# Kernel optimization log

Hardware: AMD Instinct MI355X
Metric: run time of the kernel (lower is better)

## Reference

```python
import jax, jax.numpy as jnp
import numpy as np

B, S, F, EMB, HID = 64, 2048, 40, 128, 256


def setup_inputs() -> dict:
    key = jax.random.key(0)
    ks = jax.random.split(key, 12)
    sc_in = 1.0 / np.sqrt(F)
    sc_h = 1.0 / np.sqrt(HID)
    n = lambda k, shape, sc: (jax.random.normal(k, shape, jnp.float32) * sc)
    return {
        "in_states": jax.random.normal(ks[0], (B, S, F), jnp.float32),
        "W_in": n(ks[1], (EMB, F), sc_in),
        "b_in": jnp.zeros((EMB,), jnp.float32),  # bias init to 0 in original
        "W_ih0": n(ks[2], (4 * HID, EMB), sc_h),
        "W_hh0": n(ks[3], (4 * HID, HID), sc_h),
        "b_ih0": n(ks[4], (4 * HID,), sc_h),
        "b_hh0": n(ks[5], (4 * HID,), sc_h),
        "W_ih1": n(ks[6], (4 * HID, HID), sc_h),
        "W_hh1": n(ks[7], (4 * HID, HID), sc_h),
        "b_ih1": n(ks[8], (4 * HID,), sc_h),
        "b_hh1": n(ks[9], (4 * HID,), sc_h),
        "W_out": n(ks[10], (1, HID), sc_h),
        "b_out": jnp.zeros((1,), jnp.float32),  # bias init to 0 in original
    }


def _lstm_layer(x, W_ih, W_hh, b_ih, b_hh):
    # x: [B, S, D_in]; returns hs: [B, S, H], final (h, c)
    Bb = x.shape[0]
    H = W_hh.shape[1]
    # Precompute input contribution for all timesteps (one big GEMM).
    gx = jnp.einsum('bsd,gd->bsg', x, W_ih) + b_ih + b_hh  # [B, S, 4H]

    def step(carry, gxt):
        h, c = carry
        g = gxt + h @ W_hh.T  # [B, 4H]
        i, f, gg, o = jnp.split(g, 4, axis=-1)  # PyTorch gate order i,f,g,o
        i = jax.nn.sigmoid(i)
        f = jax.nn.sigmoid(f)
        gg = jnp.tanh(gg)
        o = jax.nn.sigmoid(o)
        c = f * c + i * gg
        h = o * jnp.tanh(c)
        return (h, c), h

    init = (jnp.zeros((Bb, H), x.dtype), jnp.zeros((Bb, H), x.dtype))
    (h, c), hs = jax.lax.scan(step, init, jnp.swapaxes(gx, 0, 1))
    return jnp.swapaxes(hs, 0, 1), (h, c)


def reference(in_states, W_in, b_in, W_ih0, W_hh0, b_ih0, b_hh0,
              W_ih1, W_hh1, b_ih1, b_hh1, W_out, b_out):
    # Input projection applied to every timestep (equivalent to per-step Linear).
    x = jnp.einsum('bsf,ef->bse', in_states, W_in) + b_in  # [B, S, EMB]
    y, _ = _lstm_layer(x, W_ih0, W_hh0, b_ih0, b_hh0)
    y, _ = _lstm_layer(y, W_ih1, W_hh1, b_ih1, b_hh1)
    out = jnp.einsum('bsh,oh->bso', y, W_out) + b_out  # [B, S, 1]
    return out[..., 0]  # [B, S], matches torch.t(outputs)
```

## Files before the change

kernel.cpp:

```cpp
#include <hip/hip_runtime.h>


#define Sz    2048
#define PIPE  4
#define NG    4
#define NJ    8

typedef __attribute__((ext_vector_type(8))) short short8;
typedef __attribute__((ext_vector_type(4))) float f32x4;

#define PUB0_U64 0
#define PUB1_U64 65536
#define CFLG_U32 262144
#define WS_U32   262176

#define HA_HI 0
#define HA_LO 8448
#define HB_HI 16896
#define HB_LO 25344
#define IN_HI 33792
#define IN_LO 36096
#define GBUF  38400
#define SMEM_BYTES 46848
#define WCOMB_OFF 16896

__device__ __forceinline__ unsigned short bf16_rne(float f) {
  unsigned u = __float_as_uint(f);
  u += 0x7FFFu + ((u >> 16) & 1u);
  return (unsigned short)(u >> 16);
}
__device__ __forceinline__ float sigm(float x) { return 1.f / (1.f + __expf(-x)); }
__device__ __forceinline__ float tanh_f(float x) { return 1.f - 2.f / (__expf(2.f * x) + 1.f); }

__device__ __forceinline__ bool load_stage(const unsigned long long* __restrict__ src,
                                           unsigned tagExp, char* hi, char* lo, int tid) {
  unsigned long long v[16];
#pragma unroll
  for (int kt = 0; kt < 8; ++kt) {
    v[kt * 2]     = __hip_atomic_load(src + kt * 512 + tid,       __ATOMIC_RELAXED, __HIP_MEMORY_SCOPE_AGENT);
    v[kt * 2 + 1] = __hip_atomic_load(src + kt * 512 + 256 + tid, __ATOMIC_RELAXED, __HIP_MEMORY_SCOPE_AGENT);
  }
  bool ok = true;
#pragma unroll
  for (int kt = 0; kt < 8; ++kt) {
#pragma unroll
    for (int hh = 0; hh < 2; ++hh) {
      unsigned long long x = v[kt * 2 + hh];
      ok &= ((unsigned)(x >> 32) == tagExp);
      unsigned pk = (unsigned)x;
      int e = tid + hh * 256;
      int m = e >> 5, col = kt * 32 + (e & 31);
      *(short*)(hi + m * 528 + col * 2) = (short)(pk >> 16);
      *(short*)(lo + m * 528 + col * 2) = (short)(pk & 0xffffu);
    }
  }
  return ok;
}

__global__ void zero_kernel(unsigned* __restrict__ ws, float* __restrict__ out) {
  int i = blockIdx.x * 256 + threadIdx.x;
  if (i < WS_U32) ws[i] = 0u;
  if (i < 64 * Sz) out[i] = 0.f;
}

__global__ __launch_bounds__(256, 1) void lstm_persist(
    const float* __restrict__ xin, const float* __restrict__ W_in,
    const float* __restrict__ b_in, const float* __restrict__ W_ih0,
    const float* __restrict__ W_hh0, const float* __restrict__ b_ih0,
    const float* __restrict__ b_hh0, const float* __restrict__ W_ih1,
    const float* __restrict__ W_hh1, const float* __restrict__ b_ih1,
    const float* __restrict__ b_hh1, const float* __restrict__ W_out,
    const float* __restrict__ b_out, float* __restrict__ out,
    unsigned* __restrict__ ws) {
  const int bx = blockIdx.x;
  const int g = bx & 7;
  if (g >= NG) return;
  const int idx = bx >> 3;
  const int layer = idx >> 3;
  const int p = idx & 7;
  const int tid = (int)threadIdx.x;
  const int w = tid >> 6;
  const int lane = tid & 63;
  const int q = lane >> 4;
  const int n16 = lane & 15;

  __shared__ __align__(16) char smem[SMEM_BYTES];

  const int row0 = w * 256 + p * 32 + n16;
  const int row1 = row0 + 16;

  short8 wf_rec[8][2];
  short8 wf_in2[8][2];
  short8 wf_cmb[2][2];
  float bias0 = 0.f, bias1 = 0.f;

  {
    const float* Wrec = layer ? W_hh1 : W_hh0;
#pragma unroll
    for (int kt = 0; kt < 8; ++kt) {
#pragma unroll
      for (int u = 0; u < 2; ++u) {
        const int row = u ? row1 : row0;
        const float* src = Wrec + (size_t)row * 256 + kt * 32 + q * 8;
        union { short8 v; unsigned short s[8]; } fr;
#pragma unroll
        for (int j = 0; j < 8; ++j) fr.s[j] = bf16_rne(src[j]);
        wf_rec[kt][u] = fr.v;
      }
    }
  }
  if (layer == 1) {
#pragma unroll
    for (int kt = 0; kt < 8; ++kt) {
#pragma unroll
      for (int u = 0; u < 2; ++u) {
        const int row = u ? row1 : row0;
        const float* src = W_ih1 + (size_t)row * 256 + kt * 32 + q * 8;
        union { short8 v; unsigned short s[8]; } fr;
#pragma unroll
        for (int j = 0; j < 8; ++j) fr.s[j] = bf16_rne(src[j]);
        wf_in2[kt][u] = fr.v;
      }
    }
    bias0 = b_ih1[row0] + b_hh1[row0];
    bias1 = b_ih1[row1] + b_hh1[row1];
  } else {
    float* wcomb = (float*)(smem + WCOMB_OFF);
    for (int i = tid; i < 128 * 40; i += 256) {
      int rl = i / 40, f = i - rl * 40;
      int gate = rl >> 5, rr = rl & 31;
      int arow = gate * 256 + p * 32 + rr;
      const float* wi = W_ih0 + (size_t)arow * 128;
      float s = 0.f;
      for (int e = 0; e < 128; ++e) s += wi[e] * W_in[e * 40 + f];
      wcomb[rl * 40 + f] = s;
    }
    __syncthreads();
#pragma unroll
    for (int kt = 0; kt < 2; ++kt) {
#pragma unroll
      for (int u = 0; u < 2; ++u) {
        int rl = w * 32 + u * 16 + n16;
        union { short8 v; unsigned short s[8]; } fr;
#pragma unroll
        for (int j = 0; j < 8; ++j) {
          int k = kt * 32 + q * 8 + j;
          fr.s[j] = (k < 40) ? bf16_rne(wcomb[rl * 40 + k]) : (unsigned short)0;
        }
        wf_cmb[kt][u] = fr.v;
      }
    }
    {
      const float* wi0 = W_ih0 + (size_t)row0 * 128;
      const float* wi1 = W_ih0 + (size_t)row1 * 128;
      float s0 = 0.f, s1 = 0.f;
      for (int e = 0; e < 128; ++e) { s0 += wi0[e] * b_in[e]; s1 += wi1[e] * b_in[e]; }
      bias0 = s0 + b_ih0[row0] + b_hh0[row0];
      bias1 = s1 + b_ih0[row1] + b_hh0[row1];
    }
    __syncthreads();
    for (int i = tid; i < 2304; i += 256) *((short*)(smem + IN_HI) + i) = 0;
    __syncthreads();
  }

  float c0 = 0.f, c1 = 0.f;
  float wo = 0.f, bo = 0.f;
  if (layer == 1) { wo = W_out[p * 32 + (tid & 31)]; bo = b_out[0]; }

  unsigned long long* const pub0 = (unsigned long long*)ws + PUB0_U64;
  unsigned long long* const pub1 = (unsigned long long*)ws + PUB1_U64;
  unsigned long long* const pubMy = layer ? pub1 : pub0;
  unsigned* const cflg = ws + CFLG_U32 + g * 8;
  float* gb = (float*)(smem + GBUF);

#pragma unroll 1
  for (int t = 0; t < Sz; ++t) {
    if (layer == 0 && tid < 160) {
      int bb = tid / 10, f4 = tid - bb * 10;
      float4 inv = *(const float4*)(xin + ((size_t)(g * 16 + bb) * Sz + t) * 40 + f4 * 4);
#pragma unroll
      for (int cc = 0; cc < 4; ++cc) {
        float f = ((const float*)&inv)[cc];
        unsigned short hb = bf16_rne(f);
        float fh = __uint_as_float((unsigned)hb << 16);
        unsigned short lb = bf16_rne(f - fh);
        int col = f4 * 4 + cc;
        *(short*)(smem + IN_HI + bb * 144 + col * 2) = (short)hb;
        *(short*)(smem + IN_LO + bb * 144 + col * 2) = (short)lb;
      }
    }

    const int slot_r = (t + PIPE - 1) % PIPE;
    const unsigned long long* srcA = pubMy + (size_t)((g * PIPE + slot_r) * NJ) * 512;
    const unsigned long long* srcB = pub0 + (size_t)((g * PIPE + (t % PIPE)) * NJ) * 512;
    const unsigned tagA = (unsigned)t;
    const unsigned tagB = (unsigned)(t + 1);
    for (;;) {
      bool ok = load_stage(srcA, tagA, smem + HA_HI, smem + HA_LO, tid);
      if (layer == 1) {
        ok &= load_stage(srcB, tagB, smem + HB_HI, smem + HB_LO, tid);
      } else if (tid < 8) {
        unsigned c = __hip_atomic_load(cflg + tid, __ATOMIC_RELAXED, __HIP_MEMORY_SCOPE_AGENT);
        ok &= ((int)c >= t - 3);
      }
      if (__syncthreads_and(ok)) break;
    }
    if (layer == 1 && tid == 0)
      __hip_atomic_store(cflg + p, (unsigned)(t + 1), __ATOMIC_RELAXED, __HIP_MEMORY_SCOPE_AGENT);

    f32x4 acc0 = {0.f, 0.f, 0.f, 0.f};
    f32x4 acc1 = {0.f, 0.f, 0.f, 0.f};
    const int arow = n16 * 528;
    const int kcol = q * 8;
#pragma unroll
    for (int kt = 0; kt < 8; ++kt) {
      short8 aH = *(const short8*)(smem + HA_HI + arow + (kt * 32 + kcol) * 2);
      short8 aL = *(const short8*)(smem + HA_LO + arow + (kt * 32 + kcol) * 2);
      acc0 = __builtin_amdgcn_mfma_f32_16x16x32_bf16(aH, wf_rec[kt][0], acc0, 0, 0, 0);
      acc0 = __builtin_amdgcn_mfma_f32_16x16x32_bf16(aL, wf_rec[kt][0], acc0, 0, 0, 0);
      acc1 = __builtin_amdgcn_mfma_f32_16x16x32_bf16(aH, wf_rec[kt][1], acc1, 0, 0, 0);
      acc1 = __builtin_amdgcn_mfma_f32_16x16x32_bf16(aL, wf_rec[kt][1], acc1, 0, 0, 0);
    }
    if (layer == 1) {
#pragma unroll
      for (int kt = 0; kt < 8; ++kt) {
        short8 aH = *(const short8*)(smem + HB_HI + arow + (kt * 32 + kcol) * 2);
        short8 aL = *(const short8*)(smem + HB_LO + arow + (kt * 32 + kcol) * 2);
        acc0 = __builtin_amdgcn_mfma_f32_16x16x32_bf16(aH, wf_in2[kt][0], acc0, 0, 0, 0);
        acc0 = __builtin_amdgcn_mfma_f32_16x16x32_bf16(aL, wf_in2[kt][0], acc0, 0, 0, 0);
        acc1 = __builtin_amdgcn_mfma_f32_16x16x32_bf16(aH, wf_in2[kt][1], acc1, 0, 0, 0);
        acc1 = __builtin_amdgcn_mfma_f32_16x16x32_bf16(aL, wf_in2[kt][1], acc1, 0, 0, 0);
      }
    } else {
      const int arow_in = n16 * 144;
#pragma unroll
      for (int kt = 0; kt < 2; ++kt) {
        short8 aH = *(const short8*)(smem + IN_HI + arow_in + (kt * 32 + kcol) * 2);
        short8 aL = *(const short8*)(smem + IN_LO + arow_in + (kt * 32 + kcol) * 2);
        acc0 = __builtin_amdgcn_mfma_f32_16x16x32_bf16(aH, wf_cmb[kt][0], acc0, 0, 0, 0);
        acc0 = __builtin_amdgcn_mfma_f32_16x16x32_bf16(aL, wf_cmb[kt][0], acc0, 0, 0, 0);
        acc1 = __builtin_amdgcn_mfma_f32_16x16x32_bf16(aH, wf_cmb[kt][1], acc1, 0, 0, 0);
        acc1 = __builtin_amdgcn_mfma_f32_16x16x32_bf16(aL, wf_cmb[kt][1], acc1, 0, 0, 0);
      }
    }

#pragma unroll
    for (int u = 0; u < 2; ++u) {
      f32x4 a = u ? acc1 : acc0;
      float bs = u ? bias1 : bias0;
#pragma unroll
      for (int r = 0; r < 4; ++r) {
        float v = a[r] + bs;
        v = (w == 2) ? tanh_f(v) : sigm(v);
        gb[w * 528 + (q * 4 + r) * 33 + u * 16 + n16] = v;
      }
    }
    __syncthreads();

    unsigned long long* dst =
        pubMy + (size_t)((g * PIPE + (t % PIPE)) * NJ + p) * 512;
    const unsigned long long tagW = ((unsigned long long)(unsigned)(t + 1)) << 32;
#pragma unroll
    for (int k = 0; k < 2; ++k) {
      int e = tid + k * 256;
      int m = e >> 5, nn = e & 31;
      float iv = gb[0 * 528 + m * 33 + nn];
      float fv = gb[1 * 528 + m * 33 + nn];
      float gv = gb[2 * 528 + m * 33 + nn];
      float ov = gb[3 * 528 + m * 33 + nn];
      float c = k ? c1 : c0;
      c = fv * c + iv * gv;
      float h = ov * tanh_f(c);
      if (k) c1 = c; else c0 = c;
      unsigned short hb = bf16_rne(h);
      float fh = __uint_as_float((unsigned)hb << 16);
      unsigned short lb = bf16_rne(h - fh);
      unsigned pk = ((unsigned)hb << 16) | (unsigned)lb;
      __hip_atomic_store(dst + e, tagW | pk, __ATOMIC_RELAXED, __HIP_MEMORY_SCOPE_AGENT);
      if (layer == 1) {
        float val = h * wo;
#pragma unroll
        for (int off = 16; off; off >>= 1) val += __shfl_down(val, off, 32);
        if (nn == 0) {
          if (p == 0) val += bo;
          atomicAdd(out + (size_t)(g * 16 + m) * Sz + t, val);
        }
      }
    }
  }
}

extern "C" void kernel_launch(void* const* d_in, const int* in_sizes, int n_in,
                              void* d_out, int out_size, void* d_ws, size_t ws_size,
                              hipStream_t stream) {
  const float* xin   = (const float*)d_in[0];
  const float* W_in  = (const float*)d_in[1];
  const float* b_in  = (const float*)d_in[2];
  const float* W_ih0 = (const float*)d_in[3];
  const float* W_hh0 = (const float*)d_in[4];
  const float* b_ih0 = (const float*)d_in[5];
  const float* b_hh0 = (const float*)d_in[6];
  const float* W_ih1 = (const float*)d_in[7];
  const float* W_hh1 = (const float*)d_in[8];
  const float* b_ih1 = (const float*)d_in[9];
  const float* b_hh1 = (const float*)d_in[10];
  const float* W_out = (const float*)d_in[11];
  const float* b_out = (const float*)d_in[12];
  float* out = (float*)d_out;
  unsigned* ws = (unsigned*)d_ws;

  zero_kernel<<<(WS_U32 + 255) / 256, 256, 0, stream>>>(ws, out);
  lstm_persist<<<128, 256, 0, stream>>>(xin, W_in, b_in, W_ih0, W_hh0, b_ih0, b_hh0,
                                        W_ih1, W_hh1, b_ih1, b_hh1, W_out, b_out,
                                        out, ws);
}
```

Baseline: 7.578 ms.

## Fuse both LSTM layers into one wavefront-skewed persistent kernel with register-level gate exchange

Replaces the separate per-layer block groups with 32 blocks of 512 threads. Each block computes both layers, with layer 1 running one step behind layer 0 so both recurrences advance in the same iteration. Gate activations are exchanged through lane shuffles instead of a shared gate buffer. Polling uses per-slice pending masks with sleep, the block's own slice is written straight to LDS, and the input for the next step is prefetched. The output projection is written to workspace and reduced by a separate kernel instead of global atomics. The trade-off is more registers per thread and a longer serial chain per step.

```diff
diff --git a/kernel.cpp b/kernel.cpp
--- a/kernel.cpp
+++ b/kernel.cpp
@@ -1,292 +1,351 @@
 #include <hip/hip_runtime.h>
 
 
-#define Sz    2048
-#define PIPE  4
-#define NG    4
-#define NJ    8
+#define Sz 2048
+#define D 4
 
 typedef __attribute__((ext_vector_type(8))) short short8;
 typedef __attribute__((ext_vector_type(4))) float f32x4;
 
-#define PUB0_U64 0
-#define PUB1_U64 65536
-#define CFLG_U32 262144
-#define WS_U32   262176
-
-#define HA_HI 0
-#define HA_LO 8448
-#define HB_HI 16896
-#define HB_LO 25344
+#define R1_U64 65536
+#define GH_WORD 262144
+#define ZERO_WORDS 262144
+
+#define H0_HI 0
+#define H0_LO 8448
+#define H1_HI 16896
+#define H1_LO 25344
 #define IN_HI 33792
 #define IN_LO 36096
-#define GBUF  38400
-#define SMEM_BYTES 46848
-#define WCOMB_OFF 16896
+#define POUT  38400
+#define SMEM_BYTES 39424
 
 __device__ __forceinline__ unsigned short bf16_rne(float f) {
   unsigned u = __float_as_uint(f);
   u += 0x7FFFu + ((u >> 16) & 1u);
   return (unsigned short)(u >> 16);
 }
-__device__ __forceinline__ float sigm(float x) { return 1.f / (1.f + __expf(-x)); }
-__device__ __forceinline__ float tanh_f(float x) { return 1.f - 2.f / (__expf(2.f * x) + 1.f); }
-
-__device__ __forceinline__ bool load_stage(const unsigned long long* __restrict__ src,
-                                           unsigned tagExp, char* hi, char* lo, int tid) {
-  unsigned long long v[16];
-#pragma unroll
-  for (int kt = 0; kt < 8; ++kt) {
-    v[kt * 2]     = __hip_atomic_load(src + kt * 512 + tid,       __ATOMIC_RELAXED, __HIP_MEMORY_SCOPE_AGENT);
-    v[kt * 2 + 1] = __hip_atomic_load(src + kt * 512 + 256 + tid, __ATOMIC_RELAXED, __HIP_MEMORY_SCOPE_AGENT);
-  }
-  bool ok = true;
-#pragma unroll
-  for (int kt = 0; kt < 8; ++kt) {
-#pragma unroll
-    for (int hh = 0; hh < 2; ++hh) {
-      unsigned long long x = v[kt * 2 + hh];
-      ok &= ((unsigned)(x >> 32) == tagExp);
-      unsigned pk = (unsigned)x;
-      int e = tid + hh * 256;
-      int m = e >> 5, col = kt * 32 + (e & 31);
-      *(short*)(hi + m * 528 + col * 2) = (short)(pk >> 16);
-      *(short*)(lo + m * 528 + col * 2) = (short)(pk & 0xffffu);
-    }
-  }
-  return ok;
-}
-
-__global__ void zero_kernel(unsigned* __restrict__ ws, float* __restrict__ out) {
-  int i = blockIdx.x * 256 + threadIdx.x;
-  if (i < WS_U32) ws[i] = 0u;
-  if (i < 64 * Sz) out[i] = 0.f;
-}
-
-__global__ __launch_bounds__(256, 1) void lstm_persist(
+__device__ __forceinline__ unsigned pk_enc(float f) {
+  unsigned short hb = bf16_rne(f);
+  float fh = __uint_as_float((unsigned)hb << 16);
+  unsigned short lb = bf16_rne(f - fh);
+  return ((unsigned)hb << 16) | (unsigned)lb;
+}
+
+__global__ void zero_ws(unsigned* __restrict__ ws) {
+  int i = blockIdx.x * 512 + threadIdx.x;
+  if (i < ZERO_WORDS) ws[i] = 0u;
+}
+
+__global__ void out_reduce(const unsigned* __restrict__ ws,
+                           const float* __restrict__ b_out, float* __restrict__ out) {
+  int idx = blockIdx.x * 512 + threadIdx.x;
+  if (idx >= 64 * Sz) return;
+  int b = idx >> 11, t = idx & 2047;
+  int g = b >> 4, m = b & 15;
+  const float* gh = (const float*)(ws + GH_WORD);
+  float s = b_out[0];
+#pragma unroll
+  for (int p = 0; p < 8; ++p)
+    s += gh[((size_t)(g * 8 + p) * Sz + t) * 16 + m];
+  out[idx] = s;
+}
+
+__global__ __launch_bounds__(512, 2) void lstm_v4(
     const float* __restrict__ xin, const float* __restrict__ W_in,
     const float* __restrict__ b_in, const float* __restrict__ W_ih0,
     const float* __restrict__ W_hh0, const float* __restrict__ b_ih0,
     const float* __restrict__ b_hh0, const float* __restrict__ W_ih1,
     const float* __restrict__ W_hh1, const float* __restrict__ b_ih1,
     const float* __restrict__ b_hh1, const float* __restrict__ W_out,
-    const float* __restrict__ b_out, float* __restrict__ out,
-    unsigned* __restrict__ ws) {
+    const float* __restrict__ b_out, unsigned* __restrict__ ws) {
   const int bx = blockIdx.x;
-  const int g = bx & 7;
-  if (g >= NG) return;
-  const int idx = bx >> 3;
-  const int layer = idx >> 3;
-  const int p = idx & 7;
+  if (bx >= 32) return;
+  const int g = bx & 3, p = bx >> 2;
   const int tid = (int)threadIdx.x;
   const int w = tid >> 6;
   const int lane = tid & 63;
   const int q = lane >> 4;
   const int n16 = lane & 15;
+  const int gidx = n16 >> 2;
+  const int c4 = n16 & 3;
 
   __shared__ __align__(16) char smem[SMEM_BYTES];
 
-  const int row0 = w * 256 + p * 32 + n16;
-  const int row1 = row0 + 16;
-
-  short8 wf_rec[8][2];
-  short8 wf_in2[8][2];
-  short8 wf_cmb[2][2];
-  float bias0 = 0.f, bias1 = 0.f;
-
+  const int mycol = p * 32 + w * 4 + c4;
+  const int myrow = gidx * 256 + mycol;
+
+  short8 wf0[8], wf1[8], wfi[8];
+#pragma unroll
+  for (int kt = 0; kt < 8; ++kt) {
+    const float* s0 = W_hh0 + (size_t)myrow * 256 + kt * 32 + q * 8;
+    const float* s1 = W_hh1 + (size_t)myrow * 256 + kt * 32 + q * 8;
+    const float* si = W_ih1 + (size_t)myrow * 256 + kt * 32 + q * 8;
+    union { short8 v; unsigned short s[8]; } f0, f1, fi;
+#pragma unroll
+    for (int j = 0; j < 8; ++j) {
+      f0.s[j] = bf16_rne(s0[j]);
+      f1.s[j] = bf16_rne(s1[j]);
+      fi.s[j] = bf16_rne(si[j]);
+    }
+    wf0[kt] = f0.v; wf1[kt] = f1.v; wfi[kt] = fi.v;
+  }
+  short8 wfc[2];
+  float bL0, bL1, wo;
   {
-    const float* Wrec = layer ? W_hh1 : W_hh0;
-#pragma unroll
-    for (int kt = 0; kt < 8; ++kt) {
-#pragma unroll
-      for (int u = 0; u < 2; ++u) {
-        const int row = u ? row1 : row0;
-        const float* src = Wrec + (size_t)row * 256 + kt * 32 + q * 8;
-        union { short8 v; unsigned short s[8]; } fr;
-#pragma unroll
-        for (int j = 0; j < 8; ++j) fr.s[j] = bf16_rne(src[j]);
-        wf_rec[kt][u] = fr.v;
-      }
-    }
-  }
-  if (layer == 1) {
-#pragma unroll
-    for (int kt = 0; kt < 8; ++kt) {
-#pragma unroll
-      for (int u = 0; u < 2; ++u) {
-        const int row = u ? row1 : row0;
-        const float* src = W_ih1 + (size_t)row * 256 + kt * 32 + q * 8;
-        union { short8 v; unsigned short s[8]; } fr;
-#pragma unroll
-        for (int j = 0; j < 8; ++j) fr.s[j] = bf16_rne(src[j]);
-        wf_in2[kt][u] = fr.v;
-      }
-    }
-    bias0 = b_ih1[row0] + b_hh1[row0];
-    bias1 = b_ih1[row1] + b_hh1[row1];
-  } else {
-    float* wcomb = (float*)(smem + WCOMB_OFF);
-    for (int i = tid; i < 128 * 40; i += 256) {
-      int rl = i / 40, f = i - rl * 40;
-      int gate = rl >> 5, rr = rl & 31;
-      int arow = gate * 256 + p * 32 + rr;
-      const float* wi = W_ih0 + (size_t)arow * 128;
+    float sv[2][8];
+#pragma unroll
+    for (int kt = 0; kt < 2; ++kt)
+#pragma unroll
+      for (int j = 0; j < 8; ++j) sv[kt][j] = 0.f;
+    float bacc = 0.f;
+    const float* wr = W_ih0 + (size_t)myrow * 128;
+    for (int e = 0; e < 128; ++e) {
+      float wv = wr[e];
+      const float* wi = W_in + e * 40;
+      bacc += wv * b_in[e];
+#pragma unroll
+      for (int j = 0; j < 8; ++j) {
+        int k0 = q * 8 + j;
+        sv[0][j] += wv * wi[k0];
+        int k1 = 32 + q * 8 + j;
+        if (k1 < 40) sv[1][j] += wv * wi[k1];
+      }
+    }
+    union { short8 v; unsigned short s[8]; } c0u, c1u;
+#pragma unroll
+    for (int j = 0; j < 8; ++j) {
+      c0u.s[j] = bf16_rne(sv[0][j]);
+      c1u.s[j] = (32 + q * 8 + j < 40) ? bf16_rne(sv[1][j]) : (unsigned short)0;
+    }
+    wfc[0] = c0u.v; wfc[1] = c1u.v;
+    bL0 = b_ih0[myrow] + b_hh0[myrow] + bacc;
+    bL1 = b_ih1[myrow] + b_hh1[myrow];
+    wo = W_out[mycol];
+  }
+
+  for (int i = tid; i < 9600; i += 512) ((int*)smem)[i] = 0;
+  __syncthreads();
+  const int bb = tid / 10, f4 = tid - (tid / 10) * 10;
+  if (tid < 160) {
+    float4 xv = *(const float4*)(xin + ((size_t)(g * 16 + bb) * Sz) * 40 + f4 * 4);
+#pragma unroll
+    for (int cc = 0; cc < 4; ++cc) {
+      unsigned pk = pk_enc(((const float*)&xv)[cc]);
+      int col = f4 * 4 + cc;
+      *(short*)(smem + IN_HI + bb * 144 + col * 2) = (short)(pk >> 16);
+      *(short*)(smem + IN_LO + bb * 144 + col * 2) = (short)(pk & 0xffffu);
+    }
+  }
+
+  float c0[4] = {0.f, 0.f, 0.f, 0.f};
+  float c1[4] = {0.f, 0.f, 0.f, 0.f};
+  unsigned long long* const ring0 = (unsigned long long*)ws;
+  unsigned long long* const ring1 = ring0 + R1_U64;
+  float* const ghout = (float*)(ws + GH_WORD);
+  float* const pout = (float*)(smem + POUT);
+  const unsigned maskInit = (0xFFu & ~(1u << p)) | ((0xFFu & ~(1u << p)) << 8);
+  const int stg_m = tid >> 5, stg_c = tid & 31;
+
+#pragma unroll 1
+  for (int t = 0; t <= Sz; ++t) {
+    float4 xv;
+    const bool hasx = (t + 1 < Sz) && (tid < 160);
+    if (hasx)
+      xv = *(const float4*)(xin + ((size_t)(g * 16 + bb) * Sz + (t + 1)) * 40 + f4 * 4);
+
+    if (t > 0) {
+      const unsigned tagE = (unsigned)t;
+      const unsigned long long* s0 =
+          ring0 + ((size_t)(g * D + ((t - 1) & 3)) * 8) * 512;
+      const unsigned long long* s1 =
+          ring1 + ((size_t)(g * D + ((t - 1) & 3)) * 8) * 512;
+      unsigned pend = maskInit;
+      int spin = 0;
+      while (pend) {
+        unsigned long long v0[8], v1[8];
+#pragma unroll
+        for (int k = 0; k < 8; ++k)
+          if (pend & (1u << k))
+            v0[k] = __hip_atomic_load(s0 + k * 512 + tid, __ATOMIC_RELAXED,
+                                      __HIP_MEMORY_SCOPE_AGENT);
+#pragma unroll
+        for (int k = 0; k < 8; ++k)
+          if (pend & (1u << (8 + k)))
+            v1[k] = __hip_atomic_load(s1 + k * 512 + tid, __ATOMIC_RELAXED,
+                                      __HIP_MEMORY_SCOPE_AGENT);
+#pragma unroll
+        for (int k = 0; k < 8; ++k) {
+          if ((pend & (1u << k)) && (unsigned)(v0[k] >> 32) == tagE) {
+            unsigned pk = (unsigned)v0[k];
+            int c = k * 32 + stg_c;
+            *(short*)(smem + H0_HI + stg_m * 528 + c * 2) = (short)(pk >> 16);
+            *(short*)(smem + H0_LO + stg_m * 528 + c * 2) = (short)(pk & 0xffffu);
+            pend &= ~(1u << k);
+          }
+          if ((pend & (1u << (8 + k))) && (unsigned)(v1[k] >> 32) == tagE) {
+            unsigned pk = (unsigned)v1[k];
+            int c = k * 32 + stg_c;
+            *(short*)(smem + H1_HI + stg_m * 528 + c * 2) = (short)(pk >> 16);
+            *(short*)(smem + H1_LO + stg_m * 528 + c * 2) = (short)(pk & 0xffffu);
+            pend &= ~(1u << (8 + k));
+          }
+        }
+        if (pend && ++spin > 2) __builtin_amdgcn_s_sleep(1);
+      }
+    }
+    __syncthreads();
+
+    if (w == 0 && lane < 16 && t >= 2) {
+      const int buf = (t - 1) & 1;
       float s = 0.f;
-      for (int e = 0; e < 128; ++e) s += wi[e] * W_in[e * 40 + f];
-      wcomb[rl * 40 + f] = s;
-    }
-    __syncthreads();
-#pragma unroll
-    for (int kt = 0; kt < 2; ++kt) {
-#pragma unroll
-      for (int u = 0; u < 2; ++u) {
-        int rl = w * 32 + u * 16 + n16;
-        union { short8 v; unsigned short s[8]; } fr;
-#pragma unroll
-        for (int j = 0; j < 8; ++j) {
-          int k = kt * 32 + q * 8 + j;
-          fr.s[j] = (k < 40) ? bf16_rne(wcomb[rl * 40 + k]) : (unsigned short)0;
-        }
-        wf_cmb[kt][u] = fr.v;
-      }
-    }
-    {
-      const float* wi0 = W_ih0 + (size_t)row0 * 128;
-      const float* wi1 = W_ih0 + (size_t)row1 * 128;
-      float s0 = 0.f, s1 = 0.f;
-      for (int e = 0; e < 128; ++e) { s0 += wi0[e] * b_in[e]; s1 += wi1[e] * b_in[e]; }
-      bias0 = s0 + b_ih0[row0] + b_hh0[row0];
-      bias1 = s1 + b_ih0[row1] + b_hh0[row1];
-    }
-    __syncthreads();
-    for (int i = tid; i < 2304; i += 256) *((short*)(smem + IN_HI) + i) = 0;
-    __syncthreads();
-  }
-
-  float c0 = 0.f, c1 = 0.f;
-  float wo = 0.f, bo = 0.f;
-  if (layer == 1) { wo = W_out[p * 32 + (tid & 31)]; bo = b_out[0]; }
-
-  unsigned long long* const pub0 = (unsigned long long*)ws + PUB0_U64;
-  unsigned long long* const pub1 = (unsigned long long*)ws + PUB1_U64;
-  unsigned long long* const pubMy = layer ? pub1 : pub0;
-  unsigned* const cflg = ws + CFLG_U32 + g * 8;
-  float* gb = (float*)(smem + GBUF);
-
-#pragma unroll 1
-  for (int t = 0; t < Sz; ++t) {
-    if (layer == 0 && tid < 160) {
-      int bb = tid / 10, f4 = tid - bb * 10;
-      float4 inv = *(const float4*)(xin + ((size_t)(g * 16 + bb) * Sz + t) * 40 + f4 * 4);
-#pragma unroll
-      for (int cc = 0; cc < 4; ++cc) {
-        float f = ((const float*)&inv)[cc];
-        unsigned short hb = bf16_rne(f);
-        float fh = __uint_as_float((unsigned)hb << 16);
-        unsigned short lb = bf16_rne(f - fh);
-        int col = f4 * 4 + cc;
-        *(short*)(smem + IN_HI + bb * 144 + col * 2) = (short)hb;
-        *(short*)(smem + IN_LO + bb * 144 + col * 2) = (short)lb;
-      }
-    }
-
-    const int slot_r = (t + PIPE - 1) % PIPE;
-    const unsigned long long* srcA = pubMy + (size_t)((g * PIPE + slot_r) * NJ) * 512;
-    const unsigned long long* srcB = pub0 + (size_t)((g * PIPE + (t % PIPE)) * NJ) * 512;
-    const unsigned tagA = (unsigned)t;
-    const unsigned tagB = (unsigned)(t + 1);
-    for (;;) {
-      bool ok = load_stage(srcA, tagA, smem + HA_HI, smem + HA_LO, tid);
-      if (layer == 1) {
-        ok &= load_stage(srcB, tagB, smem + HB_HI, smem + HB_LO, tid);
-      } else if (tid < 8) {
-        unsigned c = __hip_atomic_load(cflg + tid, __ATOMIC_RELAXED, __HIP_MEMORY_SCOPE_AGENT);
-        ok &= ((int)c >= t - 3);
-      }
-      if (__syncthreads_and(ok)) break;
-    }
-    if (layer == 1 && tid == 0)
-      __hip_atomic_store(cflg + p, (unsigned)(t + 1), __ATOMIC_RELAXED, __HIP_MEMORY_SCOPE_AGENT);
+#pragma unroll
+      for (int ww = 0; ww < 8; ++ww) s += pout[buf * 32 * 4 / 4];
+      s = 0.f;
+#pragma unroll
+      for (int ww = 0; ww < 8; ++ww) s += ((float*)(smem + POUT))[buf * 128 + ww * 16 + lane];
+      ghout[((size_t)(g * 8 + p) * Sz + (t - 2)) * 16 + lane] = s;
+    }
 
     f32x4 acc0 = {0.f, 0.f, 0.f, 0.f};
     f32x4 acc1 = {0.f, 0.f, 0.f, 0.f};
-    const int arow = n16 * 528;
-    const int kcol = q * 8;
+    if (t < Sz) {
+#pragma unroll
+      for (int kt = 0; kt < 2; ++kt) {
+        short8 aH = *(const short8*)(smem + IN_HI + n16 * 144 + (kt * 32 + q * 8) * 2);
+        short8 aL = *(const short8*)(smem + IN_LO + n16 * 144 + (kt * 32 + q * 8) * 2);
+        acc0 = __builtin_amdgcn_mfma_f32_16x16x32_bf16(aH, wfc[kt], acc0, 0, 0, 0);
+        acc0 = __builtin_amdgcn_mfma_f32_16x16x32_bf16(aL, wfc[kt], acc0, 0, 0, 0);
+      }
+    }
 #pragma unroll
     for (int kt = 0; kt < 8; ++kt) {
-      short8 aH = *(const short8*)(smem + HA_HI + arow + (kt * 32 + kcol) * 2);
-      short8 aL = *(const short8*)(smem + HA_LO + arow + (kt * 32 + kcol) * 2);
-      acc0 = __builtin_amdgcn_mfma_f32_16x16x32_bf16(aH, wf_rec[kt][0], acc0, 0, 0, 0);
-      acc0 = __builtin_amdgcn_mfma_f32_16x16x32_bf16(aL, wf_rec[kt][0], acc0, 0, 0, 0);
-      acc1 = __builtin_amdgcn_mfma_f32_16x16x32_bf16(aH, wf_rec[kt][1], acc1, 0, 0, 0);
-      acc1 = __builtin_amdgcn_mfma_f32_16x16x32_bf16(aL, wf_rec[kt][1], acc1, 0, 0, 0);
-    }
-    if (layer == 1) {
-#pragma unroll
-      for (int kt = 0; kt < 8; ++kt) {
-        short8 aH = *(const short8*)(smem + HB_HI + arow + (kt * 32 + kcol) * 2);
-        short8 aL = *(const short8*)(smem + HB_LO + arow + (kt * 32 + kcol) * 2);
-        acc0 = __builtin_amdgcn_mfma_f32_16x16x32_bf16(aH, wf_in2[kt][0], acc0, 0, 0, 0);
-        acc0 = __builtin_amdgcn_mfma_f32_16x16x32_bf16(aL, wf_in2[kt][0], acc0, 0, 0, 0);
-        acc1 = __builtin_amdgcn_mfma_f32_16x16x32_bf16(aH, wf_in2[kt][1], acc1, 0, 0, 0);
-        acc1 = __builtin_amdgcn_mfma_f32_16x16x32_bf16(aL, wf_in2[kt][1], acc1, 0, 0, 0);
-      }
-    } else {
-      const int arow_in = n16 * 144;
-#pragma unroll
-      for (int kt = 0; kt < 2; ++kt) {
-        short8 aH = *(const short8*)(smem + IN_HI + arow_in + (kt * 32 + kcol) * 2);
-        short8 aL = *(const short8*)(smem + IN_LO + arow_in + (kt * 32 + kcol) * 2);
-        acc0 = __builtin_amdgcn_mfma_f32_16x16x32_bf16(aH, wf_cmb[kt][0], acc0, 0, 0, 0);
-        acc0 = __builtin_amdgcn_mfma_f32_16x16x32_bf16(aL, wf_cmb[kt][0], acc0, 0, 0, 0);
-        acc1 = __builtin_amdgcn_mfma_f32_16x16x32_bf16(aH, wf_cmb[kt][1], acc1, 0, 0, 0);
-        acc1 = __builtin_amdgcn_mfma_f32_16x16x32_bf16(aL, wf_cmb[kt][1], acc1, 0, 0, 0);
-      }
-    }
-
-#pragma unroll
-    for (int u = 0; u < 2; ++u) {
-      f32x4 a = u ? acc1 : acc0;
-      float bs = u ? bias1 : bias0;
+      short8 aH0 = *(const short8*)(smem + H0_HI + n16 * 528 + (kt * 32 + q * 8) * 2);
+      short8 aL0 = *(const short8*)(smem + H0_LO + n16 * 528 + (kt * 32 + q * 8) * 2);
+      if (t < Sz) {
+        acc0 = __builtin_amdgcn_mfma_f32_16x16x32_bf16(aH0, wf0[kt], acc0, 0, 0, 0);
+        acc0 = __builtin_amdgcn_mfma_f32_16x16x32_bf16(aL0, wf0[kt], acc0, 0, 0, 0);
+      }
+      if (t > 0) {
+        acc1 = __builtin_amdgcn_mfma_f32_16x16x32_bf16(aH0, wfi[kt], acc1, 0, 0, 0);
+        acc1 = __builtin_amdgcn_mfma_f32_16x16x32_bf16(aL0, wfi[kt], acc1, 0, 0, 0);
+        short8 aH1 = *(const short8*)(smem + H1_HI + n16 * 528 + (kt * 32 + q * 8) * 2);
+        short8 aL1 = *(const short8*)(smem + H1_LO + n16 * 528 + (kt * 32 + q * 8) * 2);
+        acc1 = __builtin_amdgcn_mfma_f32_16x16x32_bf16(aH1, wf1[kt], acc1, 0, 0, 0);
+        acc1 = __builtin_amdgcn_mfma_f32_16x16x32_bf16(aL1, wf1[kt], acc1, 0, 0, 0);
+      }
+    }
+    __syncthreads();
+
+    const unsigned long long tagW = ((unsigned long long)(unsigned)(t + 1)) << 32;
+    const bool b0 = gidx & 1, b1 = gidx & 2;
+    const float sc = (gidx == 2) ? 2.f : 1.f;
+
+    if (t < Sz) {
+      unsigned pk0[4];
 #pragma unroll
       for (int r = 0; r < 4; ++r) {
-        float v = a[r] + bs;
-        v = (w == 2) ? tanh_f(v) : sigm(v);
-        gb[w * 528 + (q * 4 + r) * 33 + u * 16 + n16] = v;
-      }
-    }
-    __syncthreads();
-
-    unsigned long long* dst =
-        pubMy + (size_t)((g * PIPE + (t % PIPE)) * NJ + p) * 512;
-    const unsigned long long tagW = ((unsigned long long)(unsigned)(t + 1)) << 32;
-#pragma unroll
-    for (int k = 0; k < 2; ++k) {
-      int e = tid + k * 256;
-      int m = e >> 5, nn = e & 31;
-      float iv = gb[0 * 528 + m * 33 + nn];
-      float fv = gb[1 * 528 + m * 33 + nn];
-      float gv = gb[2 * 528 + m * 33 + nn];
-      float ov = gb[3 * 528 + m * 33 + nn];
-      float c = k ? c1 : c0;
-      c = fv * c + iv * gv;
-      float h = ov * tanh_f(c);
-      if (k) c1 = c; else c0 = c;
-      unsigned short hb = bf16_rne(h);
-      float fh = __uint_as_float((unsigned)hb << 16);
-      unsigned short lb = bf16_rne(h - fh);
-      unsigned pk = ((unsigned)hb << 16) | (unsigned)lb;
-      __hip_atomic_store(dst + e, tagW | pk, __ATOMIC_RELAXED, __HIP_MEMORY_SCOPE_AGENT);
-      if (layer == 1) {
-        float val = h * wo;
-#pragma unroll
-        for (int off = 16; off; off >>= 1) val += __shfl_down(val, off, 32);
-        if (nn == 0) {
-          if (p == 0) val += bo;
-          atomicAdd(out + (size_t)(g * 16 + m) * Sz + t, val);
-        }
-      }
-    }
+        float a = acc0[r] + bL0;
+        float y = 1.f / (1.f + __expf(-a * sc));
+        float v = fmaf(y, sc, 1.f - sc);
+        float t1 = __shfl_xor(v, 4, 64);
+        float t2 = __shfl_xor(v, 8, 64);
+        float t3 = __shfl_xor(t1, 8, 64);
+        float pi = b1 ? (b0 ? t3 : t2) : (b0 ? t1 : v);
+        float pf = b1 ? (b0 ? t2 : t3) : (b0 ? v : t1);
+        float pg = b1 ? (b0 ? t1 : v) : (b0 ? t3 : t2);
+        float po = b1 ? (b0 ? v : t1) : (b0 ? t2 : t3);
+        float c = pf * c0[r] + pi * pg;
+        c0[r] = c;
+        float th = 2.f / (1.f + __expf(-2.f * c)) - 1.f;
+        pk0[r] = pk_enc(po * th);
+      }
+      unsigned long long* dst0 = ring0 + ((size_t)(g * D + (t & 3)) * 8 + p) * 512;
+      if (gidx == 0) {
+#pragma unroll
+        for (int r = 0; r < 4; ++r)
+          __hip_atomic_store(dst0 + (q * 4 + r) * 32 + w * 4 + c4, tagW | pk0[r],
+                             __ATOMIC_RELAXED, __HIP_MEMORY_SCOPE_AGENT);
+      } else if (gidx == 1) {
+#pragma unroll
+        for (int r = 0; r < 4; ++r) {
+          int m = q * 4 + r;
+          *(short*)(smem + H0_HI + m * 528 + mycol * 2) = (short)(pk0[r] >> 16);
+          *(short*)(smem + H0_LO + m * 528 + mycol * 2) = (short)(pk0[r] & 0xffffu);
+        }
+      }
+    }
+    {
+      float h1v[4] = {0.f, 0.f, 0.f, 0.f};
+      unsigned pk1[4] = {0u, 0u, 0u, 0u};
+      if (t > 0) {
+#pragma unroll
+        for (int r = 0; r < 4; ++r) {
+          float a = acc1[r] + bL1;
+          float y = 1.f / (1.f + __expf(-a * sc));
+          float v = fmaf(y, sc, 1.f - sc);
+          float t1 = __shfl_xor(v, 4, 64);
+          float t2 = __shfl_xor(v, 8, 64);
+          float t3 = __shfl_xor(t1, 8, 64);
+          float pi = b1 ? (b0 ? t3 : t2) : (b0 ? t1 : v);
+          float pf = b1 ? (b0 ? t2 : t3) : (b0 ? v : t1);
+          float pg = b1 ? (b0 ? t1 : v) : (b0 ? t3 : t2);
+          float po = b1 ? (b0 ? v : t1) : (b0 ? t2 : t3);
+          float c = pf * c1[r] + pi * pg;
+          c1[r] = c;
+          float th = 2.f / (1.f + __expf(-2.f * c)) - 1.f;
+          h1v[r] = po * th;
+          pk1[r] = pk_enc(h1v[r]);
+        }
+      }
+      if (t < Sz) {
+        unsigned long long* dst1 = ring1 + ((size_t)(g * D + (t & 3)) * 8 + p) * 512;
+        if (gidx == 0) {
+#pragma unroll
+          for (int r = 0; r < 4; ++r)
+            __hip_atomic_store(dst1 + (q * 4 + r) * 32 + w * 4 + c4, tagW | pk1[r],
+                               __ATOMIC_RELAXED, __HIP_MEMORY_SCOPE_AGENT);
+        } else if (gidx == 1) {
+#pragma unroll
+          for (int r = 0; r < 4; ++r) {
+            int m = q * 4 + r;
+            *(short*)(smem + H1_HI + m * 528 + mycol * 2) = (short)(pk1[r] >> 16);
+            *(short*)(smem + H1_LO + m * 528 + mycol * 2) = (short)(pk1[r] & 0xffffu);
+          }
+        }
+      }
+      if (t > 0) {
+        float vr[4];
+#pragma unroll
+        for (int r = 0; r < 4; ++r) {
+          float v = h1v[r] * wo;
+          v += __shfl_xor(v, 1, 64);
+          v += __shfl_xor(v, 2, 64);
+          vr[r] = v;
+        }
+        if (n16 == 12) {
+#pragma unroll
+          for (int r = 0; r < 4; ++r)
+            ((float*)(smem + POUT))[(t & 1) * 128 + w * 16 + q * 4 + r] = vr[r];
+        }
+      }
+    }
+    if (hasx) {
+#pragma unroll
+      for (int cc = 0; cc < 4; ++cc) {
+        unsigned pk = pk_enc(((const float*)&xv)[cc]);
+        int col = f4 * 4 + cc;
+        *(short*)(smem + IN_HI + bb * 144 + col * 2) = (short)(pk >> 16);
+        *(short*)(smem + IN_LO + bb * 144 + col * 2) = (short)(pk & 0xffffu);
+      }
+    }
+  }
+  __syncthreads();
+  if (w == 0 && lane < 16) {
+    float s = 0.f;
+#pragma unroll
+    for (int ww = 0; ww < 8; ++ww) s += ((float*)(smem + POUT))[(Sz & 1) * 128 + ww * 16 + lane];
+    ghout[((size_t)(g * 8 + p) * Sz + (Sz - 1)) * 16 + lane] = s;
   }
 }
 
@@ -309,8 +368,8 @@
   float* out = (float*)d_out;
   unsigned* ws = (unsigned*)d_ws;
 
-  zero_kernel<<<(WS_U32 + 255) / 256, 256, 0, stream>>>(ws, out);
-  lstm_persist<<<128, 256, 0, stream>>>(xin, W_in, b_in, W_ih0, W_hh0, b_ih0, b_hh0,
-                                        W_ih1, W_hh1, b_ih1, b_hh1, W_out, b_out,
-                                        out, ws);
-}
+  zero_ws<<<(ZERO_WORDS + 511) / 512, 512, 0, stream>>>(ws);
+  lstm_v4<<<32, 512, 0, stream>>>(xin, W_in, b_in, W_ih0, W_hh0, b_ih0, b_hh0,
+                                  W_ih1, W_hh1, b_ih1, b_hh1, W_out, b_out, ws);
+  out_reduce<<<(64 * Sz + 511) / 512, 512, 0, stream>>>(ws, b_out, out);
+}
```

New measurement: 11.85 ms. 56.3% more time.
